# Performance work log

Measured on AMD Instinct MI355X. Metric: run time of the kernel, lower is better.

Reference implementation:

```python
import jax, jax.numpy as jnp
import numpy as np
import math

N = 10000      # num nodes
DEG = 3        # base avg out-degree of random directed graph
D = 128        # d_model
H = 8          # heads
C = D // H     # head dim
L = 2          # num_layers
HOPS = 2       # num_hops


def _build_attn_window(rng):
    # random directed base graph
    E0 = N * DEG
    s0 = rng.integers(0, N, E0).astype(np.int64)
    d0 = rng.integers(0, N, E0).astype(np.int64)
    # to_undirected + coalesce
    s = np.concatenate([s0, d0]); d = np.concatenate([d0, s0])
    key = np.unique(s * N + d)
    s, d = key // N, key % N
    # add self loops (as in _get_attn_window) and coalesce
    loops = np.arange(N, dtype=np.int64)
    key = np.unique(np.concatenate([loops * N + loops, s * N + d]))
    s, d = key // N, key % N
    # base adjacency in CSR-like form grouped by source
    order = np.argsort(s, kind='stable')
    bss, bsd = s[order], d[order]
    outdeg = np.bincount(bss, minlength=N)
    indptr = np.concatenate([[0], np.cumsum(outdeg)])
    # k_hop = A; for _ in range(HOPS-1): k_hop = k_hop @ A   (boolean sparse product)
    cs, cd = s.copy(), d.copy()
    for _ in range(HOPS - 1):
        counts = outdeg[cd]
        total = int(counts.sum())
        new_s = np.repeat(cs, counts)
        starts = np.repeat(indptr[cd], counts)
        offs = np.arange(total, dtype=np.int64) - np.repeat(
            np.concatenate([[0], np.cumsum(counts)])[:-1], counts)
        new_d = bsd[starts + offs]
        key = np.unique(new_s * N + new_d)
        cs, cd = key // N, key % N
    return np.stack([cs, cd]).astype(np.int64)  # [2, E2] (src, dst)


def setup_inputs() -> dict:
    rng = np.random.default_rng(0)
    aw = _build_attn_window(rng)
    key = jax.random.key(0)
    ks = jax.random.split(key, 10)
    sc = 1.0 / math.sqrt(D)
    x = jax.random.normal(ks[0], (N, D), jnp.float32)
    Wq = jax.random.normal(ks[1], (L, D, D), jnp.float32) * sc
    Wk = jax.random.normal(ks[2], (L, D, D), jnp.float32) * sc
    Wv = jax.random.normal(ks[3], (L, D, D), jnp.float32) * sc
    Ws = jax.random.normal(ks[4], (L, D, D), jnp.float32) * sc
    bq = jax.random.normal(ks[5], (L, D), jnp.float32) * 0.01
    bk = jax.random.normal(ks[6], (L, D), jnp.float32) * 0.01
    bv = jax.random.normal(ks[7], (L, D), jnp.float32) * 0.01
    bs = jax.random.normal(ks[8], (L, D), jnp.float32) * 0.01
    return {"x": x, "Wq": Wq, "bq": bq, "Wk": Wk, "bk": bk,
            "Wv": Wv, "bv": bv, "Ws": Ws, "bs": bs,
            "attn_window": jnp.asarray(aw)}


def _segment_softmax(logits, seg):
    # logits: [E, H], seg: [E] destination node ids (every node has a self loop)
    m = jax.ops.segment_max(logits, seg, num_segments=N)
    e = jnp.exp(logits - m[seg])
    z = jax.ops.segment_sum(e, seg, num_segments=N)
    return e / z[seg]


def _transformer_conv(h, wq, bq_, wk, bk_, wv, bv_, ws, bs_, src, dst):
    # PyG TransformerConv (concat=True, root_weight=True, beta=False, eval mode)
    q = (h @ wq + bq_).reshape(N, H, C)
    k = (h @ wk + bk_).reshape(N, H, C)
    v = (h @ wv + bv_).reshape(N, H, C)
    logits = jnp.einsum('ehc,ehc->eh', q[dst], k[src]) * (1.0 / math.sqrt(C))
    alpha = _segment_softmax(logits, dst)                       # [E, H]
    agg = jax.ops.segment_sum(alpha[:, :, None] * v[src], dst,  # [N, H, C]
                              num_segments=N)
    return agg.reshape(N, D) + h @ ws + bs_


def reference(x, Wq, bq, Wk, bk, Wv, bv, Ws, bs, attn_window):
    src, dst = attn_window[0], attn_window[1]
    h = x
    for l in range(L - 1):
        h = jax.nn.relu(h + _transformer_conv(
            h, Wq[l], bq[l], Wk[l], bk[l], Wv[l], bv[l], Ws[l], bs[l], src, dst))
    l = L - 1
    h = h + _transformer_conv(
        h, Wq[l], bq[l], Wk[l], bk[l], Wv[l], bv[l], Ws[l], bs[l], src, dst)
    return h
```

## Files before the change

### kernel.cpp

```cpp
#include <hip/hip_runtime.h>
#include <hip/hip_bf16.h>

typedef __hip_bfloat16 bf16;
typedef __attribute__((ext_vector_type(8))) short bf16x8v;
typedef __attribute__((ext_vector_type(4))) float f32x4v;
typedef __attribute__((ext_vector_type(2))) float f32x2v;

#define N_NODES 10000
#define DMODEL  128
#define NHEADS  8
#define CHEAD   16


#ifndef __has_builtin
#define __has_builtin(x) 0
#endif
#if __has_builtin(__builtin_amdgcn_cvt_pk_f32_fp8) && \
    __has_builtin(__builtin_amdgcn_cvt_pk_fp8_f32)
#define FP8_HW 1
#else
#define FP8_HW 0
#endif

__device__ __forceinline__ float bf2f(unsigned u) {
    union { unsigned i; float f; } c; c.i = u << 16; return c.f;
}
__device__ __forceinline__ unsigned short f2bf_bits(float f) {
    bf16 b = __float2bfloat16(f);
    return *(unsigned short*)&b;
}

__device__ __forceinline__ unsigned char f2fp8(float f) {
#if FP8_HW
    int p = __builtin_amdgcn_cvt_pk_fp8_f32(f, f, 0, false);
    return (unsigned char)(p & 0xff);
#else
    _Float16 hf = (_Float16)f;
    unsigned short u = *reinterpret_cast<unsigned short*>(&hf);
    unsigned s = (u >> 8) & 0x80u;
    unsigned mag = u & 0x7fffu;
    unsigned t = mag + 0x3Fu + ((mag >> 7) & 1u);
    int v = (int)(t >> 7) - 0x40;
    if (v < 0) v = 0;
    if (v > 0x7e) v = 0x7e;
    return (unsigned char)(s | (unsigned)v);
#endif
}
__device__ __forceinline__ void fp8x4_to_f32(unsigned w, float* f) {
#if FP8_HW
    f32x2v lo = __builtin_amdgcn_cvt_pk_f32_fp8((int)w, false);
    f32x2v hi = __builtin_amdgcn_cvt_pk_f32_fp8((int)w, true);
    f[0] = lo[0]; f[1] = lo[1]; f[2] = hi[0]; f[3] = hi[1];
#else
    #pragma unroll
    for (int i = 0; i < 4; ++i) {
        unsigned b = (w >> (8 * i)) & 0xffu;
        unsigned h = ((b & 0x80u) << 8) | (((b & 0x7fu) << 7) + 0x2000u);
        h = (b & 0x7fu) ? h : ((b & 0x80u) << 8);
        unsigned short us = (unsigned short)h;
        _Float16 f16 = *reinterpret_cast<_Float16*>(&us);
        f[i] = (float)f16;
    }
#endif
}

__global__ __launch_bounds__(256) void gemm_qkvs(
    const void* __restrict__ Ain, int a_is_bf16,
    const float* __restrict__ Wq, const float* __restrict__ Wk,
    const float* __restrict__ Wv, const float* __restrict__ Ws,
    const float* __restrict__ bq, const float* __restrict__ bk,
    const float* __restrict__ bv, const float* __restrict__ bs,
    int welem, int belem,
    float* __restrict__ qo, unsigned char* __restrict__ ko,
    bf16* __restrict__ vo, float* __restrict__ hso,
    const int* __restrict__ aw, int E,
    int* __restrict__ rowptr, int* __restrict__ nbr)
{
    __shared__ unsigned short As[64][136];
    __shared__ unsigned short Bs[128][68];
    __shared__ int nz;

    const int tid = threadIdx.x;

    if (E > 0) {
        if (tid == 0) nz = 0;
        __syncthreads();
        int W = 4096;
        if (W > 2 * E) W = 2 * E;
        int any = 0;
        for (int w = 1 + 2 * tid; w < W; w += 2 * (int)blockDim.x)
            any |= aw[w];
        if (any) atomicOr(&nz, 1);
        __syncthreads();
        const int is64 = (nz == 0);

        const int gid = (blockIdx.y * gridDim.x + blockIdx.x) * blockDim.x
                      + tid;
        const int gtot = gridDim.x * gridDim.y * blockDim.x;
        if (gid == 0) rowptr[N_NODES] = E;
        for (int e = gid; e < E; e += gtot) {
            int s  = is64 ? aw[2 * e] : aw[e];
            if (s < 0) s = 0;
            if (s >= N_NODES) s = N_NODES - 1;
            int sp = (e == 0) ? -1 : (is64 ? aw[2 * (e - 1)] : aw[e - 1]);
            for (int r = sp + 1; r <= s; ++r) rowptr[r] = e;
            if (e == E - 1)
                for (int r = s + 1; r < N_NODES; ++r) rowptr[r] = E;
            int d = is64 ? aw[2 * (E + e)] : aw[E + e];
            if (d < 0) d = 0;
            if (d >= N_NODES) d = N_NODES - 1;
            nbr[e] = d;
        }
        __syncthreads();
    }

    const int cb    = blockIdx.x;
    const int row0  = blockIdx.y * 64;
    const int mat   = cb >> 1;
    const float* W    = (mat == 0) ? Wq : (mat == 1) ? Wk
                      : (mat == 2) ? Wv : Ws;
    const float* bias = (mat == 0) ? bq : (mat == 1) ? bk
                      : (mat == 2) ? bv : bs;
    const int colW0 = (cb & 1) * 64;

    if (a_is_bf16) {
        const unsigned short* A = (const unsigned short*)Ain;
        #pragma unroll
        for (int i = 0; i < 4; ++i) {
            int idx = tid + i * 256;
            int row = idx >> 4, k8 = idx & 15;
            int grow = row0 + row;
            uint4 u = make_uint4(0u, 0u, 0u, 0u);
            if (grow < N_NODES)
                u = *(const uint4*)&A[grow * DMODEL + k8 * 8];
            *(uint4*)&As[row][k8 * 8] = u;
        }
    } else {
        const float* A = (const float*)Ain;
        #pragma unroll
        for (int i = 0; i < 8; ++i) {
            int idx = tid + i * 256;
            int row = idx >> 5, k4 = idx & 31;
            int grow = row0 + row;
            float4 av = make_float4(0.f, 0.f, 0.f, 0.f);
            if (grow < N_NODES)
                av = *(const float4*)&A[grow * DMODEL + k4 * 4];
            ushort4 p;
            p.x = f2bf_bits(av.x); p.y = f2bf_bits(av.y);
            p.z = f2bf_bits(av.z); p.w = f2bf_bits(av.w);
            *(ushort4*)&As[row][k4 * 4] = p;
        }
    }
    #pragma unroll
    for (int i = 0; i < 8; ++i) {
        int idx = tid + i * 256;
        int kk = idx >> 4, n4 = idx & 15;
        float4 wv = *(const float4*)&W[welem + kk * DMODEL + colW0 + n4 * 4];
        ushort4 p;
        p.x = f2bf_bits(wv.x); p.y = f2bf_bits(wv.y);
        p.z = f2bf_bits(wv.z); p.w = f2bf_bits(wv.w);
        *(ushort4*)&Bs[kk][n4 * 4] = p;
    }
    __syncthreads();

    const int wave = tid >> 6, lane = tid & 63;
    const int ln = lane & 15, quad = lane >> 4;
    const int ncol = wave * 16 + ln;

    f32x4v acc[4];
    #pragma unroll
    for (int mt = 0; mt < 4; ++mt) acc[mt] = (f32x4v){0.f, 0.f, 0.f, 0.f};

    #pragma unroll
    for (int ks = 0; ks < 4; ++ks) {
        const int kb = ks * 32 + quad * 8;
        bf16x8v bfv;
        #pragma unroll
        for (int j = 0; j < 8; ++j) bfv[j] = (short)Bs[kb + j][ncol];
        #pragma unroll
        for (int mt = 0; mt < 4; ++mt) {
            bf16x8v afv = *(const bf16x8v*)&As[mt * 16 + ln][kb];
            acc[mt] = __builtin_amdgcn_mfma_f32_16x16x32_bf16(
                afv, bfv, acc[mt], 0, 0, 0);
        }
    }

    const float bcol = bias[belem + colW0 + ncol];
    #pragma unroll
    for (int mt = 0; mt < 4; ++mt) {
        #pragma unroll
        for (int r = 0; r < 4; ++r) {
            int row = row0 + mt * 16 + quad * 4 + r;
            if (row >= N_NODES) continue;
            float val = acc[mt][r] + bcol;
            int elo = row * DMODEL + colW0 + ncol;
            if (mat == 0)      qo[elo] = val;
            else if (mat == 3) hso[elo] = val;
            else if (mat == 1) ko[elo] = f2fp8(val);
            else               vo[elo] = __float2bfloat16(val);
        }
    }
}

__global__ __launch_bounds__(128) void attn_fused(
    const float* __restrict__ q, const unsigned char* __restrict__ k,
    const bf16* __restrict__ v, const float* __restrict__ hs,
    const float* __restrict__ hin_f,
    const unsigned short* __restrict__ hin_b,
    const int* __restrict__ rowptr, const int* __restrict__ nbr,
    float* __restrict__ out, unsigned short* __restrict__ outb,
    int relu_flag)
{
    __shared__ float part[16][132];
    __shared__ float lzw[2][8];

    const int wv = threadIdx.x >> 6;
    const int l = threadIdx.x & 63;
    const int h = l & 7, slot = l >> 3;

    const int d = blockIdx.x;

    float qf[16];
    const float* qp = q + d * DMODEL + h * CHEAD;
    #pragma unroll
    for (int i = 0; i < 4; ++i) {
        float4 t4 = *(const float4*)(qp + i * 4);
        qf[i * 4 + 0] = t4.x; qf[i * 4 + 1] = t4.y;
        qf[i * 4 + 2] = t4.z; qf[i * 4 + 3] = t4.w;
    }

    const int e0 = rowptr[d], e1 = rowptr[d + 1];
    float zacc = 0.f;
    float acc[16];
    #pragma unroll
    for (int j = 0; j < 16; ++j) acc[j] = 0.f;

    const int start = e0 + wv * 8;
    {
        int eg = start + slot;
        bool pad_cur = !(eg < e1);
        int s_cur = pad_cur ? d : nbr[eg];
        uint4 kc = *(const uint4*)(k + s_cur * DMODEL + h * CHEAD);
        const uint4* vp = (const uint4*)(v + s_cur * DMODEL + h * CHEAD);
        uint4 vc0 = vp[0], vc1 = vp[1];

        for (int base = start; base < e1; base += 16) {
            int en = base + 16 + slot;
            bool pad_nxt = !(en < e1);
            int s_nxt = pad_nxt ? d : nbr[en];
            uint4 kn = *(const uint4*)(k + s_nxt * DMODEL + h * CHEAD);
            const uint4* vpn = (const uint4*)(v + s_nxt * DMODEL + h * CHEAD);
            uint4 vn0 = vpn[0], vn1 = vpn[1];

            const unsigned* kw = (const unsigned*)&kc;
            float dot = 0.f;
            #pragma unroll
            for (int w = 0; w < 4; ++w) {
                float kf[4];
                fp8x4_to_f32(kw[w], kf);
                dot += qf[w * 4 + 0] * kf[0];
                dot += qf[w * 4 + 1] * kf[1];
                dot += qf[w * 4 + 2] * kf[2];
                dot += qf[w * 4 + 3] * kf[3];
            }
            float p = pad_cur ? -3.0e38f : fminf(dot * 0.25f, 60.f);
            float pe = __expf(p);
            zacc += pe;

            const unsigned* vw0 = (const unsigned*)&vc0;
            const unsigned* vw1 = (const unsigned*)&vc1;
            #pragma unroll
            for (int w = 0; w < 4; ++w) {
                acc[2 * w + 0] += pe * bf2f(vw0[w] & 0xffffu);
                acc[2 * w + 1] += pe * bf2f(vw0[w] >> 16);
                acc[8 + 2 * w + 0] += pe * bf2f(vw1[w] & 0xffffu);
                acc[8 + 2 * w + 1] += pe * bf2f(vw1[w] >> 16);
            }

            kc = kn; vc0 = vn0; vc1 = vn1; pad_cur = pad_nxt;
        }
    }

    float z = zacc;
    z += __shfl_xor(z, 8);
    z += __shfl_xor(z, 16);
    z += __shfl_xor(z, 32);
    if (l < 8) lzw[wv][l] = z;

    const int p = wv * 8 + slot;
    #pragma unroll
    for (int i = 0; i < 4; ++i)
        *(float4*)&part[p][h * CHEAD + i * 4] =
            make_float4(acc[i * 4 + 0], acc[i * 4 + 1],
                        acc[i * 4 + 2], acc[i * 4 + 3]);
    __syncthreads();

    float ax = 0.f, ay = 0.f;
    #pragma unroll
    for (int i = 0; i < 16; ++i) {
        float2 t = *(const float2*)&part[i][2 * l];
        ax += t.x; ay += t.y;
    }
    float zt = lzw[0][l >> 3] + lzw[1][l >> 3];
    float inv = (zt > 0.f) ? (1.f / zt) : 0.f;

    const bool do_f32 = (out  != 0) && (wv == 0);
    const bool do_bf  = (outb != 0) && (wv == 1);
    if (do_f32 || do_bf) {
        int idx = d * DMODEL + 2 * l;
        float2 hsv = *(const float2*)(hs + idx);
        float2 hiv;
        if (hin_f) {
            hiv = *(const float2*)(hin_f + idx);
        } else {
            unsigned u = *(const unsigned*)(hin_b + idx);
            hiv.x = bf2f(u & 0xffffu);
            hiv.y = bf2f(u >> 16);
        }
        float2 o;
        o.x = ax * inv + hsv.x + hiv.x;
        o.y = ay * inv + hsv.y + hiv.y;
        if (relu_flag) { o.x = fmaxf(o.x, 0.f); o.y = fmaxf(o.y, 0.f); }
        if (do_f32) *(float2*)(out + idx) = o;
        if (do_bf) {
            unsigned pk = f2bf_bits(o.x) | ((unsigned)f2bf_bits(o.y) << 16);
            *(unsigned*)&outb[idx] = pk;
        }
    }
}

extern "C" void kernel_launch(void* const* d_in, const int* in_sizes, int n_in,
                              void* d_out, int out_size, void* d_ws, size_t ws_size,
                              hipStream_t stream) {
    const float* x  = (const float*)d_in[0];
    const float* Wq = (const float*)d_in[1];
    const float* bq = (const float*)d_in[2];
    const float* Wk = (const float*)d_in[3];
    const float* bk = (const float*)d_in[4];
    const float* Wv = (const float*)d_in[5];
    const float* bv = (const float*)d_in[6];
    const float* Ws = (const float*)d_in[7];
    const float* bs = (const float*)d_in[8];
    const int*   aw = (const int*)d_in[9];
    const int E = in_sizes[9] / 2;

    char* ws = (char*)d_ws;
    size_t off = 0;
    float* qb = (float*)(ws + off);  off += (size_t)N_NODES * DMODEL * 4;
    unsigned char* kb = (unsigned char*)(ws + off);
    off += (size_t)N_NODES * DMODEL;
    off = (off + 255) & ~(size_t)255;
    bf16*  vb = (bf16*)(ws + off);   off += (size_t)N_NODES * DMODEL * 2;
    float* hsb = (float*)(ws + off); off += (size_t)N_NODES * DMODEL * 4;
    unsigned short* h1b = (unsigned short*)(ws + off);
    off += (size_t)N_NODES * DMODEL * 2;
    int* rowptr = (int*)(ws + off);  off += ((size_t)N_NODES + 2) * 4;
    int* nbr    = (int*)(ws + off);  off += (size_t)E * 4;

    dim3 ggrid(8, (N_NODES + 63) / 64);

    gemm_qkvs<<<ggrid, 256, 0, stream>>>(x, 0, Wq, Wk, Wv, Ws,
                                         bq, bk, bv, bs, 0, 0,
                                         qb, kb, vb, hsb, aw, E, rowptr, nbr);
    attn_fused<<<N_NODES, 128, 0, stream>>>(qb, kb, vb, hsb, x,
                                            (const unsigned short*)0,
                                            rowptr, nbr,
                                            (float*)0, h1b, 1);
    gemm_qkvs<<<ggrid, 256, 0, stream>>>(h1b, 1, Wq, Wk, Wv, Ws,
                                         bq, bk, bv, bs,
                                         DMODEL * DMODEL, DMODEL,
                                         qb, kb, vb, hsb, aw, 0, rowptr, nbr);
    attn_fused<<<N_NODES, 128, 0, stream>>>(qb, kb, vb, hsb,
                                            (const float*)0, h1b,
                                            rowptr, nbr,
                                            (float*)d_out,
                                            (unsigned short*)0, 0);
}
```

Before: 148.9 us.

## Pre-transpose weights to bf16, pre-convert x, and pack two nodes per attention block

Adds a prep kernel that converts x to bf16 and stores all weights transposed in bf16 (n-major). The GEMM then loads B tiles with vector copies and reads MFMA B fragments as contiguous 16-byte LDS loads instead of eight strided scalar reads. The attention kernel now processes two destination nodes per 256-thread block, halving the block count. The cost is an extra kernel launch plus extra traffic to write and read the converted x and weights.

```diff
diff --git a/kernel.cpp b/kernel.cpp
--- a/kernel.cpp
+++ b/kernel.cpp
@@ -64,20 +64,55 @@
 #endif
 }
 
-__global__ __launch_bounds__(256) void gemm_qkvs(
-    const void* __restrict__ Ain, int a_is_bf16,
+__global__ __launch_bounds__(256) void prep(
+    const float* __restrict__ x,
     const float* __restrict__ Wq, const float* __restrict__ Wk,
     const float* __restrict__ Wv, const float* __restrict__ Ws,
+    unsigned short* __restrict__ xb, unsigned short* __restrict__ wt)
+{
+    const int gid = blockIdx.x * 256 + threadIdx.x;
+
+    if (gid < 2 * 4 * 128 * 16) {
+        const int k8 = gid & 15, n = (gid >> 4) & 127,
+                  mat = (gid >> 11) & 3, l = gid >> 13;
+        const float* W = (mat == 0) ? Wq : (mat == 1) ? Wk
+                       : (mat == 2) ? Wv : Ws;
+        const float* src = W + (size_t)l * DMODEL * DMODEL + n;
+        unsigned short t[8];
+        #pragma unroll
+        for (int j = 0; j < 8; ++j)
+            t[j] = f2bf_bits(src[(k8 * 8 + j) * DMODEL]);
+        unsigned short* dst =
+            wt + (((size_t)(l * 4 + mat) * 128 + n) * 128 + k8 * 8);
+        *(ushort4*)dst       = make_ushort4(t[0], t[1], t[2], t[3]);
+        *(ushort4*)(dst + 4) = make_ushort4(t[4], t[5], t[6], t[7]);
+    }
+
+    const int tot = N_NODES * DMODEL / 4;
+    const int gtot = gridDim.x * 256;
+    for (int i = gid; i < tot; i += gtot) {
+        float4 a = *(const float4*)&x[i * 4];
+        ushort4 p;
+        p.x = f2bf_bits(a.x); p.y = f2bf_bits(a.y);
+        p.z = f2bf_bits(a.z); p.w = f2bf_bits(a.w);
+        *(ushort4*)&xb[i * 4] = p;
+    }
+}
+
+__global__ __launch_bounds__(256) void gemm_qkvs(
+    const unsigned short* __restrict__ Ain,
+    const unsigned short* __restrict__ wt,
+    int layer,
     const float* __restrict__ bq, const float* __restrict__ bk,
     const float* __restrict__ bv, const float* __restrict__ bs,
-    int welem, int belem,
+    int belem,
     float* __restrict__ qo, unsigned char* __restrict__ ko,
     bf16* __restrict__ vo, float* __restrict__ hso,
     const int* __restrict__ aw, int E,
     int* __restrict__ rowptr, int* __restrict__ nbr)
 {
     __shared__ unsigned short As[64][136];
-    __shared__ unsigned short Bs[128][68];
+    __shared__ unsigned short Bs[64][136];
     __shared__ int nz;
 
     const int tid = threadIdx.x;
@@ -117,49 +152,30 @@
     const int cb    = blockIdx.x;
     const int row0  = blockIdx.y * 64;
     const int mat   = cb >> 1;
-    const float* W    = (mat == 0) ? Wq : (mat == 1) ? Wk
-                      : (mat == 2) ? Wv : Ws;
     const float* bias = (mat == 0) ? bq : (mat == 1) ? bk
                       : (mat == 2) ? bv : bs;
     const int colW0 = (cb & 1) * 64;
 
-    if (a_is_bf16) {
-        const unsigned short* A = (const unsigned short*)Ain;
+    #pragma unroll
+    for (int i = 0; i < 4; ++i) {
+        int idx = tid + i * 256;
+        int row = idx >> 4, k8 = idx & 15;
+        int grow = row0 + row;
+        uint4 u = make_uint4(0u, 0u, 0u, 0u);
+        if (grow < N_NODES)
+            u = *(const uint4*)&Ain[grow * DMODEL + k8 * 8];
+        *(uint4*)&As[row][k8 * 8] = u;
+    }
+    {
+        const unsigned short* Wbase =
+            wt + ((size_t)(layer * 4 + mat) * 128 + colW0) * 128;
         #pragma unroll
         for (int i = 0; i < 4; ++i) {
             int idx = tid + i * 256;
             int row = idx >> 4, k8 = idx & 15;
-            int grow = row0 + row;
-            uint4 u = make_uint4(0u, 0u, 0u, 0u);
-            if (grow < N_NODES)
-                u = *(const uint4*)&A[grow * DMODEL + k8 * 8];
-            *(uint4*)&As[row][k8 * 8] = u;
-        }
-    } else {
-        const float* A = (const float*)Ain;
-        #pragma unroll
-        for (int i = 0; i < 8; ++i) {
-            int idx = tid + i * 256;
-            int row = idx >> 5, k4 = idx & 31;
-            int grow = row0 + row;
-            float4 av = make_float4(0.f, 0.f, 0.f, 0.f);
-            if (grow < N_NODES)
-                av = *(const float4*)&A[grow * DMODEL + k4 * 4];
-            ushort4 p;
-            p.x = f2bf_bits(av.x); p.y = f2bf_bits(av.y);
-            p.z = f2bf_bits(av.z); p.w = f2bf_bits(av.w);
-            *(ushort4*)&As[row][k4 * 4] = p;
-        }
-    }
-    #pragma unroll
-    for (int i = 0; i < 8; ++i) {
-        int idx = tid + i * 256;
-        int kk = idx >> 4, n4 = idx & 15;
-        float4 wv = *(const float4*)&W[welem + kk * DMODEL + colW0 + n4 * 4];
-        ushort4 p;
-        p.x = f2bf_bits(wv.x); p.y = f2bf_bits(wv.y);
-        p.z = f2bf_bits(wv.z); p.w = f2bf_bits(wv.w);
-        *(ushort4*)&Bs[kk][n4 * 4] = p;
+            *(uint4*)&Bs[row][k8 * 8] =
+                *(const uint4*)&Wbase[row * 128 + k8 * 8];
+        }
     }
     __syncthreads();
 
@@ -174,9 +190,7 @@
     #pragma unroll
     for (int ks = 0; ks < 4; ++ks) {
         const int kb = ks * 32 + quad * 8;
-        bf16x8v bfv;
-        #pragma unroll
-        for (int j = 0; j < 8; ++j) bfv[j] = (short)Bs[kb + j][ncol];
+        bf16x8v bfv = *(const bf16x8v*)&Bs[ncol][kb];
         #pragma unroll
         for (int mt = 0; mt < 4; ++mt) {
             bf16x8v afv = *(const bf16x8v*)&As[mt * 16 + ln][kb];
@@ -202,7 +216,7 @@
     }
 }
 
-__global__ __launch_bounds__(128) void attn_fused(
+__global__ __launch_bounds__(256) void attn_fused(
     const float* __restrict__ q, const unsigned char* __restrict__ k,
     const bf16* __restrict__ v, const float* __restrict__ hs,
     const float* __restrict__ hin_f,
@@ -211,14 +225,16 @@
     float* __restrict__ out, unsigned short* __restrict__ outb,
     int relu_flag)
 {
-    __shared__ float part[16][132];
-    __shared__ float lzw[2][8];
-
-    const int wv = threadIdx.x >> 6;
-    const int l = threadIdx.x & 63;
+    __shared__ float part[2][16][132];
+    __shared__ float lzw[2][2][8];
+
+    const int half = threadIdx.x >> 7;
+    const int t = threadIdx.x & 127;
+    const int wv = t >> 6;
+    const int l = t & 63;
     const int h = l & 7, slot = l >> 3;
 
-    const int d = blockIdx.x;
+    const int d = blockIdx.x * 2 + half;
 
     float qf[16];
     const float* qp = q + d * DMODEL + h * CHEAD;
@@ -285,12 +301,12 @@
     z += __shfl_xor(z, 8);
     z += __shfl_xor(z, 16);
     z += __shfl_xor(z, 32);
-    if (l < 8) lzw[wv][l] = z;
+    if (l < 8) lzw[half][wv][l] = z;
 
     const int p = wv * 8 + slot;
     #pragma unroll
     for (int i = 0; i < 4; ++i)
-        *(float4*)&part[p][h * CHEAD + i * 4] =
+        *(float4*)&part[half][p][h * CHEAD + i * 4] =
             make_float4(acc[i * 4 + 0], acc[i * 4 + 1],
                         acc[i * 4 + 2], acc[i * 4 + 3]);
     __syncthreads();
@@ -298,10 +314,10 @@
     float ax = 0.f, ay = 0.f;
     #pragma unroll
     for (int i = 0; i < 16; ++i) {
-        float2 t = *(const float2*)&part[i][2 * l];
-        ax += t.x; ay += t.y;
-    }
-    float zt = lzw[0][l >> 3] + lzw[1][l >> 3];
+        float2 t2 = *(const float2*)&part[half][i][2 * l];
+        ax += t2.x; ay += t2.y;
+    }
+    float zt = lzw[half][0][l >> 3] + lzw[half][1][l >> 3];
     float inv = (zt > 0.f) ? (1.f / zt) : 0.f;
 
     const bool do_f32 = (out  != 0) && (wv == 0);
@@ -354,25 +370,27 @@
     float* hsb = (float*)(ws + off); off += (size_t)N_NODES * DMODEL * 4;
     unsigned short* h1b = (unsigned short*)(ws + off);
     off += (size_t)N_NODES * DMODEL * 2;
+    unsigned short* xb = (unsigned short*)(ws + off);
+    off += (size_t)N_NODES * DMODEL * 2;
+    unsigned short* wt = (unsigned short*)(ws + off);
+    off += (size_t)2 * 4 * DMODEL * DMODEL * 2;
     int* rowptr = (int*)(ws + off);  off += ((size_t)N_NODES + 2) * 4;
     int* nbr    = (int*)(ws + off);  off += (size_t)E * 4;
 
     dim3 ggrid(8, (N_NODES + 63) / 64);
 
-    gemm_qkvs<<<ggrid, 256, 0, stream>>>(x, 0, Wq, Wk, Wv, Ws,
-                                         bq, bk, bv, bs, 0, 0,
+    prep<<<512, 256, 0, stream>>>(x, Wq, Wk, Wv, Ws, xb, wt);
+    gemm_qkvs<<<ggrid, 256, 0, stream>>>(xb, wt, 0, bq, bk, bv, bs, 0,
                                          qb, kb, vb, hsb, aw, E, rowptr, nbr);
-    attn_fused<<<N_NODES, 128, 0, stream>>>(qb, kb, vb, hsb, x,
-                                            (const unsigned short*)0,
-                                            rowptr, nbr,
-                                            (float*)0, h1b, 1);
-    gemm_qkvs<<<ggrid, 256, 0, stream>>>(h1b, 1, Wq, Wk, Wv, Ws,
-                                         bq, bk, bv, bs,
-                                         DMODEL * DMODEL, DMODEL,
+    attn_fused<<<N_NODES / 2, 256, 0, stream>>>(qb, kb, vb, hsb, x,
+                                                (const unsigned short*)0,
+                                                rowptr, nbr,
+                                                (float*)0, h1b, 1);
+    gemm_qkvs<<<ggrid, 256, 0, stream>>>(h1b, wt, 1, bq, bk, bv, bs, DMODEL,
                                          qb, kb, vb, hsb, aw, 0, rowptr, nbr);
-    attn_fused<<<N_NODES, 128, 0, stream>>>(qb, kb, vb, hsb,
-                                            (const float*)0, h1b,
-                                            rowptr, nbr,
-                                            (float*)d_out,
-                                            (unsigned short*)0, 0);
-}
+    attn_fused<<<N_NODES / 2, 256, 0, stream>>>(qb, kb, vb, hsb,
+                                                (const float*)0, h1b,
+                                                rowptr, nbr,
+                                                (float*)d_out,
+                                                (unsigned short*)0, 0);
+}
```

New measurement: 150.6 us. Within noise of the previous version (+1.1%).
